# Performance work log

Measured on AMD Instinct MI355X. Metric: run time of the kernel, lower is better.

The kernel has to match this reference:

```python
import jax, jax.numpy as jnp
import numpy as np

FEATURES_DIM = 100000
NUM_FIELDS = 39
EMBED_DIM = 64
DIM_INT = (2, 3)
RANK = (32, 32)
BATCH = 8192


def setup_inputs() -> dict:
    key = jax.random.key(0)
    ks = jax.random.split(key, 6)
    x = jax.random.randint(ks[0], (BATCH, NUM_FIELDS), 0, FEATURES_DIM)
    embed_table = jax.random.normal(ks[1], (FEATURES_DIM, EMBED_DIM), dtype=jnp.float32) * 0.01
    linear_w = jax.random.normal(ks[2], (FEATURES_DIM, 1), dtype=jnp.float32) * 0.01
    linear_bias = jnp.zeros((1,), dtype=jnp.float32)
    # trunc_normal_(std=0.01) approximated by clipped normal
    W0 = jnp.clip(jax.random.normal(ks[3], (DIM_INT[0], RANK[0], NUM_FIELDS), dtype=jnp.float32) * 0.01, -0.02, 0.02)
    W1 = jnp.clip(jax.random.normal(ks[4], (DIM_INT[1], RANK[1], NUM_FIELDS), dtype=jnp.float32) * 0.01, -0.02, 0.02)
    return {"x": x, "embed_table": embed_table, "linear_w": linear_w,
            "linear_bias": linear_bias, "W0": W0, "W1": W1}


def _calc_cross(W, emb):
    # W: (l, j, k) = (dim_int, rank, num_fields); emb: (b, k, i) = (batch, fields, embed)
    # dot_products[b,i,j,l] = sum_k W[l,j,k] * emb[b,k,i]
    dp = jnp.einsum('ljk,bki->bijl', W, emb)          # (b, embed, rank, dim_int)
    prod_over_l = jnp.prod(dp, axis=3)                # (b, embed, rank)
    return jnp.sum(prod_over_l, axis=(1, 2))          # (b,)


def reference(x, embed_table, linear_w, linear_bias, W0, W1):
    emb = embed_table[x]                              # (b, fields, embed)
    lin = jnp.sum(linear_w[x], axis=1) + linear_bias  # (b, 1)
    ret = lin[:, 0] + _calc_cross(W0, emb) + _calc_cross(W1, emb)
    return ret                                        # (b,)
```

## Files before the change

kernel.cpp:

```cpp
#include <hip/hip_runtime.h>
#include <hip/hip_bf16.h>

#define BATCH    8192
#define NF       39
#define ED       64
#define RANK     32
#define SPW      2
#define KST      72

typedef _Float16 half8  __attribute__((ext_vector_type(8)));
typedef float    f32x16 __attribute__((ext_vector_type(16)));

__global__ __launch_bounds__(256, 3) void tfm_kernel(
    const int*   __restrict__ x,
    const float* __restrict__ embed,
    const float* __restrict__ linw,
    const float* __restrict__ lbias,
    const float* __restrict__ W0,
    const float* __restrict__ W1,
    float*       __restrict__ out)
{
    __shared__ __align__(16) _Float16 Es[4][ED][KST];

    const int t    = threadIdx.x;
    const int lane = t & 63;
    const int w    = t >> 6;
    const int s0   = (blockIdx.x * 4 + w) * SPW;

    const float bias = lbias[0];
    const int j  = lane & 31;
    const int kh = lane >> 5;

    int xv[SPW];
#pragma unroll
    for (int si = 0; si < SPW; ++si)
        xv[si] = (lane < NF) ? x[(s0 + si) * NF + lane] : 0;

    float lv[SPW];
#pragma unroll
    for (int si = 0; si < SPW; ++si)
        lv[si] = (lane < NF) ? linw[xv[si]] : 0.0f;

    half8 wf[5][3];
#pragma unroll
    for (int l = 0; l < 5; ++l) {
        const float* base = (l < 2) ? (W0 + (l * RANK + j) * NF)
                                    : (W1 + ((l - 2) * RANK + j) * NF);
#pragma unroll
        for (int kc = 0; kc < 3; ++kc)
#pragma unroll
            for (int e = 0; e < 8; ++e) {
                int k = kc * 16 + kh * 8 + e;
                wf[l][kc][e] = (k < NF) ? (_Float16)base[k] : (_Float16)0.0f;
            }
    }

#pragma unroll
    for (int si = 0; si < SPW; ++si) {
        float r[NF];
#pragma unroll
        for (int k = 0; k < NF; ++k) {
            int xi = __builtin_amdgcn_readlane(xv[si], k);
            r[k] = embed[(size_t)xi * ED + lane];
        }

#pragma unroll
        for (int c6 = 0; c6 < 6; ++c6) {
            half8 hh;
#pragma unroll
            for (int e = 0; e < 8; ++e) {
                int k = c6 * 8 + e;
                hh[e] = (k < NF) ? (_Float16)r[k] : (_Float16)0.0f;
            }
            *(half8*)&Es[w][lane][c6 * 8] = hh;
        }

        float ssum = lv[si];

#pragma unroll
        for (int tile = 0; tile < 2; ++tile) {
            const int c = tile * 32 + j;
            half8 bf[3];
#pragma unroll
            for (int kc = 0; kc < 3; ++kc)
                bf[kc] = *(const half8*)&Es[w][c][kc * 16 + kh * 8];

            {
                f32x16 a0, a1;
#pragma unroll
                for (int e = 0; e < 16; ++e) { a0[e] = 0.0f; a1[e] = 0.0f; }
#pragma unroll
                for (int kc = 0; kc < 3; ++kc) {
                    a0 = __builtin_amdgcn_mfma_f32_32x32x16_f16(wf[0][kc], bf[kc], a0, 0, 0, 0);
                    a1 = __builtin_amdgcn_mfma_f32_32x32x16_f16(wf[1][kc], bf[kc], a1, 0, 0, 0);
                }
#pragma unroll
                for (int e = 0; e < 16; ++e) ssum += a0[e] * a1[e];
            }
            {
                f32x16 c0, c1, c2;
#pragma unroll
                for (int e = 0; e < 16; ++e) { c0[e] = 0.0f; c1[e] = 0.0f; c2[e] = 0.0f; }
#pragma unroll
                for (int kc = 0; kc < 3; ++kc) {
                    c0 = __builtin_amdgcn_mfma_f32_32x32x16_f16(wf[2][kc], bf[kc], c0, 0, 0, 0);
                    c1 = __builtin_amdgcn_mfma_f32_32x32x16_f16(wf[3][kc], bf[kc], c1, 0, 0, 0);
                    c2 = __builtin_amdgcn_mfma_f32_32x32x16_f16(wf[4][kc], bf[kc], c2, 0, 0, 0);
                }
#pragma unroll
                for (int e = 0; e < 16; ++e) ssum += c0[e] * c1[e] * c2[e];
            }
        }

#pragma unroll
        for (int off = 32; off > 0; off >>= 1) ssum += __shfl_down(ssum, off, 64);
        if (lane == 0) out[s0 + si] = ssum + bias;
    }
}

extern "C" void kernel_launch(void* const* d_in, const int* in_sizes, int n_in,
                              void* d_out, int out_size, void* d_ws, size_t ws_size,
                              hipStream_t stream) {
    const int*   x     = (const int*)  d_in[0];
    const float* embed = (const float*)d_in[1];
    const float* linw  = (const float*)d_in[2];
    const float* lbias = (const float*)d_in[3];
    const float* W0    = (const float*)d_in[4];
    const float* W1    = (const float*)d_in[5];
    float*       out   = (float*)d_out;

    tfm_kernel<<<BATCH / (4 * SPW), 256, 0, stream>>>(x, embed, linw, lbias, W0, W1, out);
}
```

Before: 102.7 us.

## Pre-pack W fragments in a prep kernel and batch embedding gathers across samples

```diff
diff --git a/kernel.cpp b/kernel.cpp
--- a/kernel.cpp
+++ b/kernel.cpp
@@ -6,21 +6,41 @@
 #define ED       64
 #define RANK     32
 #define SPW      2
-#define KST      72
+#define KST      48
+#define NFRAG    15
 
 typedef _Float16 half8  __attribute__((ext_vector_type(8)));
 typedef float    f32x16 __attribute__((ext_vector_type(16)));
+
+__global__ void prep_w(const float* __restrict__ W0,
+                       const float* __restrict__ W1,
+                       half8* __restrict__ wsW) {
+    int d = blockIdx.x * 256 + threadIdx.x;
+    if (d >= NFRAG * 64) return;
+    int fid  = d >> 6;
+    int lane = d & 63;
+    int l = fid / 3, kc = fid % 3;
+    int j = lane & 31, kh = lane >> 5;
+    const float* base = (l < 2) ? (W0 + (l * RANK + j) * NF)
+                                : (W1 + ((l - 2) * RANK + j) * NF);
+    half8 h;
+#pragma unroll
+    for (int e = 0; e < 8; ++e) {
+        int k = kc * 16 + kh * 8 + e;
+        h[e] = (k < NF) ? (_Float16)base[k] : (_Float16)0.0f;
+    }
+    wsW[d] = h;
+}
 
 __global__ __launch_bounds__(256, 3) void tfm_kernel(
     const int*   __restrict__ x,
     const float* __restrict__ embed,
     const float* __restrict__ linw,
     const float* __restrict__ lbias,
-    const float* __restrict__ W0,
-    const float* __restrict__ W1,
+    const half8* __restrict__ wsW,
     float*       __restrict__ out)
 {
-    __shared__ __align__(16) _Float16 Es[4][ED][KST];
+    __shared__ __align__(16) _Float16 Es[4][SPW][ED][KST];
 
     const int t    = threadIdx.x;
     const int lane = t & 63;
@@ -43,38 +63,35 @@
 
     half8 wf[5][3];
 #pragma unroll
-    for (int l = 0; l < 5; ++l) {
-        const float* base = (l < 2) ? (W0 + (l * RANK + j) * NF)
-                                    : (W1 + ((l - 2) * RANK + j) * NF);
+    for (int l = 0; l < 5; ++l)
 #pragma unroll
         for (int kc = 0; kc < 3; ++kc)
+            wf[l][kc] = wsW[(l * 3 + kc) * 64 + lane];
+
+    float r[SPW][NF];
 #pragma unroll
-            for (int e = 0; e < 8; ++e) {
-                int k = kc * 16 + kh * 8 + e;
-                wf[l][kc][e] = (k < NF) ? (_Float16)base[k] : (_Float16)0.0f;
-            }
-    }
-
-#pragma unroll
-    for (int si = 0; si < SPW; ++si) {
-        float r[NF];
+    for (int si = 0; si < SPW; ++si)
 #pragma unroll
         for (int k = 0; k < NF; ++k) {
             int xi = __builtin_amdgcn_readlane(xv[si], k);
-            r[k] = embed[(size_t)xi * ED + lane];
+            r[si][k] = embed[(size_t)xi * ED + lane];
         }
 
+#pragma unroll
+    for (int si = 0; si < SPW; ++si)
 #pragma unroll
         for (int c6 = 0; c6 < 6; ++c6) {
             half8 hh;
 #pragma unroll
             for (int e = 0; e < 8; ++e) {
                 int k = c6 * 8 + e;
-                hh[e] = (k < NF) ? (_Float16)r[k] : (_Float16)0.0f;
+                hh[e] = (k < NF) ? (_Float16)r[si][k] : (_Float16)0.0f;
             }
-            *(half8*)&Es[w][lane][c6 * 8] = hh;
+            *(half8*)&Es[w][si][lane][c6 * 8] = hh;
         }
 
+#pragma unroll
+    for (int si = 0; si < SPW; ++si) {
         float ssum = lv[si];
 
 #pragma unroll
@@ -83,7 +100,7 @@
             half8 bf[3];
 #pragma unroll
             for (int kc = 0; kc < 3; ++kc)
-                bf[kc] = *(const half8*)&Es[w][c][kc * 16 + kh * 8];
+                bf[kc] = *(const half8*)&Es[w][si][c][kc * 16 + kh * 8];
 
             {
                 f32x16 a0, a1;
@@ -128,6 +145,8 @@
     const float* W0    = (const float*)d_in[4];
     const float* W1    = (const float*)d_in[5];
     float*       out   = (float*)d_out;
+    half8*       wsW   = (half8*)d_ws;
 
-    tfm_kernel<<<BATCH / (4 * SPW), 256, 0, stream>>>(x, embed, linw, lbias, W0, W1, out);
+    prep_w<<<(NFRAG * 64 + 255) / 256, 256, 0, stream>>>(W0, W1, wsW);
+    tfm_kernel<<<BATCH / (4 * SPW), 256, 0, stream>>>(x, embed, linw, lbias, wsW, out);
 }
```

New measurement: 99.20 us. 1.03x faster.
